# Kernel tuning notes

Hardware: AMD Instinct MI355X
Metric: run time of the kernel (lower is better)

The kernel has to match this reference:

```python
import jax, jax.numpy as jnp
import numpy as np

B, L, D, H = 2, 2048, 1024, 16
Dh = D // H            # 64
DIL = 2                # dilation
WIN = 256              # window_size
HID = 4 * D            # ffn hidden (mlp_ratio=4.0)
EPS = 1e-5             # LayerNorm eps (torch default)


def _layernorm(x, w, b):
    m = jnp.mean(x, axis=-1, keepdims=True)
    v = jnp.mean(jnp.square(x - m), axis=-1, keepdims=True)
    return (x - m) * jax.lax.rsqrt(v + EPS) * w + b


def _dilated_mask(L):
    i = jnp.arange(L)[:, None]
    j = jnp.arange(L)[None, :]
    d = i - j
    return (jnp.remainder(d, DIL) == 0) & (jnp.abs(d) <= WIN) & (j <= i)  # [L,L] bool, True=allowed


def setup_inputs() -> dict:
    key = jax.random.key(0)
    ks = jax.random.split(key, 16)
    s = 0.02
    return {
        "x": jax.random.normal(ks[0], (B, L, D), jnp.float32),
        "norm1_w": jnp.ones((D,), jnp.float32),
        "norm1_b": jnp.zeros((D,), jnp.float32),
        "qkv_w": jax.random.normal(ks[1], (D, 3 * D), jnp.float32) * s,
        "qkv_b": jnp.zeros((3 * D,), jnp.float32),
        "out_w": jax.random.normal(ks[2], (D, D), jnp.float32) * s,
        "out_b": jnp.zeros((D,), jnp.float32),
        "norm2_w": jnp.ones((D,), jnp.float32),
        "norm2_b": jnp.zeros((D,), jnp.float32),
        "ffn_w1": jax.random.normal(ks[3], (D, HID), jnp.float32) * s,
        "ffn_b1": jnp.zeros((HID,), jnp.float32),
        "ffn_w2": jax.random.normal(ks[4], (HID, D), jnp.float32) * s,
        "ffn_b2": jnp.zeros((D,), jnp.float32),
    }


def reference(x, norm1_w, norm1_b, qkv_w, qkv_b, out_w, out_b,
              norm2_w, norm2_b, ffn_w1, ffn_b1, ffn_w2, ffn_b2):
    # pre-norm dilated attention block
    xn = _layernorm(x, norm1_w, norm1_b)
    qkv = xn @ qkv_w + qkv_b                         # [B,L,3D]
    q, k, v = jnp.split(qkv, 3, axis=-1)
    to_h = lambda t: t.reshape(B, L, H, Dh).transpose(0, 2, 1, 3)  # [B,H,L,Dh]
    qh, kh, vh = to_h(q), to_h(k), to_h(v)

    scale = 1.0 / jnp.sqrt(jnp.float32(Dh))
    scores = jnp.einsum('bhqd,bhkd->bhqk', qh, kh) * scale  # [B,H,L,L]
    allowed = _dilated_mask(L)                               # [L,L]
    scores = jnp.where(allowed[None, None], scores, jnp.float32(-1e30))
    p = jax.nn.softmax(scores, axis=-1)
    o = jnp.einsum('bhqk,bhkd->bhqd', p, vh)                 # [B,H,L,Dh]
    o = o.transpose(0, 2, 1, 3).reshape(B, L, D)
    attn_out = o @ out_w + out_b

    y = x + attn_out                                          # residual (dropout=0)
    h = _layernorm(y, norm2_w, norm2_b)
    h = jax.nn.gelu(h @ ffn_w1 + ffn_b1, approximate=False) @ ffn_w2 + ffn_b2
    return y + h
```

## Files before the change

### kernel.cpp

```cpp
#include <hip/hip_runtime.h>
#include <math.h>

#define BB 2
#define LL 2048
#define DD 1024
#define HH 16
#define DH 64
#define HID 4096
#define MROWS (BB*LL)

typedef __attribute__((ext_vector_type(8))) short bf16x8;
typedef __attribute__((ext_vector_type(4))) float f32x4;

__device__ __forceinline__ unsigned short f2bf(float f) {
    unsigned u = __builtin_bit_cast(unsigned, f);
    unsigned r = u + 0x7fffu + ((u >> 16) & 1u);
    return (unsigned short)(r >> 16);
}

__device__ __forceinline__ void ldsload16(const void* g, void* l) {
    __builtin_amdgcn_global_load_lds(
        (const __attribute__((address_space(1))) unsigned int*)g,
        (__attribute__((address_space(3))) unsigned int*)l,
        16, 0, 0);
}

__global__ __launch_bounds__(256) void convT_kernel(const float* __restrict__ in,
                                                    unsigned short* __restrict__ out,
                                                    int K, int N) {
    __shared__ float tile[64][65];
    int kt = blockIdx.y << 6, nt = blockIdx.x << 6;
    int t = threadIdx.x;
    int tr = t >> 4;
    int tc = (t & 15) << 2;
    #pragma unroll
    for (int i = 0; i < 4; ++i) {
        float4 v = *reinterpret_cast<const float4*>(&in[(size_t)(kt + i*16 + tr) * N + nt + tc]);
        tile[i*16 + tr][tc+0] = v.x;
        tile[i*16 + tr][tc+1] = v.y;
        tile[i*16 + tr][tc+2] = v.z;
        tile[i*16 + tr][tc+3] = v.w;
    }
    __syncthreads();
    #pragma unroll
    for (int i = 0; i < 4; ++i) {
        int n = i*16 + tr;
        ushort4 o4;
        o4.x = f2bf(tile[tc+0][n]);
        o4.y = f2bf(tile[tc+1][n]);
        o4.z = f2bf(tile[tc+2][n]);
        o4.w = f2bf(tile[tc+3][n]);
        *reinterpret_cast<ushort4*>(&out[(size_t)(nt + n) * K + kt + tc]) = o4;
    }
}

__global__ __launch_bounds__(256) void ln_kernel(const float* __restrict__ in,
                                                 const float* __restrict__ w,
                                                 const float* __restrict__ b,
                                                 unsigned short* __restrict__ out) {
    int row = blockIdx.x;
    const float* x = in + (size_t)row * DD;
    unsigned short* o = out + (size_t)row * DD;
    int t = threadIdx.x;
    float4 v = reinterpret_cast<const float4*>(x)[t];
    float s  = v.x + v.y + v.z + v.w;
    float ss = v.x*v.x + v.y*v.y + v.z*v.z + v.w*v.w;
    #pragma unroll
    for (int off = 32; off > 0; off >>= 1) {
        s  += __shfl_down(s,  off, 64);
        ss += __shfl_down(ss, off, 64);
    }
    __shared__ float red[8];
    int wid = t >> 6, lane = t & 63;
    if (lane == 0) { red[wid] = s; red[4 + wid] = ss; }
    __syncthreads();
    if (t == 0) {
        float S  = red[0] + red[1] + red[2] + red[3];
        float SS = red[4] + red[5] + red[6] + red[7];
        float mean = S / DD;
        float var  = SS / DD - mean * mean;
        red[0] = mean;
        red[1] = rsqrtf(var + 1e-5f);
    }
    __syncthreads();
    float mean = red[0], rstd = red[1];
    float4 wv = reinterpret_cast<const float4*>(w)[t];
    float4 bv = reinterpret_cast<const float4*>(b)[t];
    ushort4 ov;
    ov.x = f2bf((v.x - mean) * rstd * wv.x + bv.x);
    ov.y = f2bf((v.y - mean) * rstd * wv.y + bv.y);
    ov.z = f2bf((v.z - mean) * rstd * wv.z + bv.z);
    ov.w = f2bf((v.w - mean) * rstd * wv.w + bv.w);
    reinterpret_cast<ushort4*>(o)[t] = ov;
}

template<int EPI>
__global__ __launch_bounds__(256) void mgemm(
    const unsigned short* __restrict__ A,
    const unsigned short* __restrict__ WT,
    const float* __restrict__ bias,
    const float* res, void* Cv,
    int M, int N, int K, int nbx)
{
    __shared__ __align__(16) unsigned char smem[49152];
    int bid = blockIdx.x;
    int nwg = gridDim.x;
    int cpx = nwg >> 3;
    int swz = (bid & 7) * cpx + (bid >> 3);
    int bn = (swz % nbx) * 128;
    int bm = (swz / nbx) * 128;
    int t = threadIdx.x, lane = t & 63, w = t >> 6;
    int wr = w >> 1, wc = w & 1;
    int l15 = lane & 15, l4 = lane >> 4;

    const unsigned short* Ap = A  + (size_t)(bm + w*32 + l15) * K + 8*l4;
    const unsigned short* Bp = WT + (size_t)(bn + w*32 + l15) * K + 8*l4;
    unsigned stoff = w*2048 + lane*16;

    f32x4 acc[4][4] = {};
    int nk = K >> 5;

    unsigned char* pb0 = smem;
    unsigned char* pb1 = smem + 16384;
    unsigned char* pb2 = smem + 32768;

    auto stage = [&](unsigned char* bs) {
        ldsload16(Ap,        bs + stoff);
        ldsload16(Ap + 16*K, bs + stoff + 1024);
        ldsload16(Bp,        bs + 8192 + stoff);
        ldsload16(Bp + 16*K, bs + 8192 + stoff + 1024);
        Ap += 32; Bp += 32;
    };

    stage(pb0);
    stage(pb1);

    for (int k = 0; k < nk; ++k) {
        if (k + 2 < nk) {
            stage(pb2);
            asm volatile("s_waitcnt vmcnt(8)\ns_barrier" ::: "memory");
        } else if (k + 2 == nk) {
            asm volatile("s_waitcnt vmcnt(4)\ns_barrier" ::: "memory");
        } else {
            asm volatile("s_waitcnt vmcnt(0)\ns_barrier" ::: "memory");
        }
        unsigned char* Asb = pb0;
        unsigned char* Bsb = pb0 + 8192;
        bf16x8 af[4], bfr[4];
        #pragma unroll
        for (int mm = 0; mm < 4; ++mm)
            af[mm] = *reinterpret_cast<const bf16x8*>(Asb + (wr*4 + mm)*1024 + lane*16);
        #pragma unroll
        for (int nn = 0; nn < 4; ++nn)
            bfr[nn] = *reinterpret_cast<const bf16x8*>(Bsb + (wc*4 + nn)*1024 + lane*16);
        #pragma unroll
        for (int mm = 0; mm < 4; ++mm)
            #pragma unroll
            for (int nn = 0; nn < 4; ++nn)
                acc[mm][nn] = __builtin_amdgcn_mfma_f32_16x16x32_bf16(af[mm], bfr[nn], acc[mm][nn], 0, 0, 0);
        asm volatile("s_waitcnt lgkmcnt(0)\ns_barrier" ::: "memory");
        unsigned char* tp = pb0; pb0 = pb1; pb1 = pb2; pb2 = tp;
    }

    #pragma unroll
    for (int mm = 0; mm < 4; ++mm) {
        int row0 = bm + wr*64 + mm*16 + l4*4;
        #pragma unroll
        for (int nn = 0; nn < 4; ++nn) {
            int col = bn + wc*64 + nn*16 + l15;
            float bi = bias[col];
            #pragma unroll
            for (int r = 0; r < 4; ++r) {
                float v = acc[mm][nn][r] + bi;
                size_t idx = (size_t)(row0 + r) * N + col;
                if (EPI == 2) {
                    ((float*)Cv)[idx] = v + res[idx];
                } else {
                    v = 0.5f * v * (1.0f + erff(v * 0.70710678118654752f));
                    ((unsigned short*)Cv)[idx] = f2bf(v);
                }
            }
        }
    }
}

template<int EPI>
__global__ __launch_bounds__(512, 2) void mgemm256(
    const unsigned short* __restrict__ A,
    const unsigned short* __restrict__ WT,
    const float* __restrict__ bias,
    void* Cv,
    unsigned short* __restrict__ vt,
    int M, int N, int K, int nbx)
{
    __shared__ __align__(16) unsigned char smem[131072];
    int bid = blockIdx.x;
    int nwg = gridDim.x;
    int cpx = nwg >> 3;
    int swz = (bid & 7) * cpx + (bid >> 3);
    int bn = (swz % nbx) * 256;
    int bm = (swz / nbx) * 256;
    int t = threadIdx.x, lane = t & 63, w = t >> 6;
    int wr = w >> 2, wc = w & 3;
    int l15 = lane & 15, l4 = lane >> 4;

    const unsigned short* Ap0 = A  + (size_t)(bm + w*16 + l15) * K + 8*l4;
    const unsigned short* Ap1 = Ap0 + (size_t)128 * K;
    const unsigned short* Bp0 = WT + (size_t)(bn + w*16 + l15) * K + 8*l4;
    const unsigned short* Bp1 = Bp0 + (size_t)128 * K;
    unsigned aoff = w*1024 + lane*16;
    int koff = 0;

    f32x4 acc[8][4] = {};
    int nk = K >> 6;

    auto stage = [&](int buf) {
        unsigned char* Asb = smem + (buf << 16);
        unsigned char* Bsb = Asb + 32768;
        ldsload16(Ap0 + koff,      Asb + aoff);
        ldsload16(Ap1 + koff,      Asb + aoff + 8192);
        ldsload16(Ap0 + koff + 32, Asb + aoff + 16384);
        ldsload16(Ap1 + koff + 32, Asb + aoff + 24576);
        ldsload16(Bp0 + koff,      Bsb + aoff);
        ldsload16(Bp1 + koff,      Bsb + aoff + 8192);
        ldsload16(Bp0 + koff + 32, Bsb + aoff + 16384);
        ldsload16(Bp1 + koff + 32, Bsb + aoff + 24576);
        koff += 64;
    };

    stage(0);
    for (int k = 0; k < nk; ++k) {
        if (k + 1 < nk) {
            stage((k + 1) & 1);
            asm volatile("s_waitcnt vmcnt(8)\ns_barrier" ::: "memory");
        } else {
            asm volatile("s_waitcnt vmcnt(0)\ns_barrier" ::: "memory");
        }
        unsigned char* Asb = smem + ((k & 1) << 16);
        unsigned char* Bsb = Asb + 32768;
        #pragma unroll
        for (int kc = 0; kc < 2; ++kc) {
            bf16x8 af[8], bfr[4];
            #pragma unroll
            for (int mm = 0; mm < 8; ++mm)
                af[mm] = *reinterpret_cast<const bf16x8*>(Asb + kc*16384 + (wr*8 + mm)*1024 + lane*16);
            #pragma unroll
            for (int nn = 0; nn < 4; ++nn)
                bfr[nn] = *reinterpret_cast<const bf16x8*>(Bsb + kc*16384 + (wc*4 + nn)*1024 + lane*16);
            #pragma unroll
            for (int mm = 0; mm < 8; ++mm)
                #pragma unroll
                for (int nn = 0; nn < 4; ++nn)
                    acc[mm][nn] = __builtin_amdgcn_mfma_f32_16x16x32_bf16(af[mm], bfr[nn], acc[mm][nn], 0, 0, 0);
        }
        asm volatile("s_waitcnt lgkmcnt(0)\ns_barrier" ::: "memory");
    }

    bool isv = (EPI == 3) && (bn >= 2048);
    #pragma unroll
    for (int mm = 0; mm < 8; ++mm) {
        int row0 = bm + wr*128 + mm*16 + l4*4;
        #pragma unroll
        for (int nn = 0; nn < 4; ++nn) {
            int col = bn + wc*64 + nn*16 + l15;
            float bi = bias[col];
            #pragma unroll
            for (int r = 0; r < 4; ++r) {
                float v = acc[mm][nn][r] + bi;
                int row = row0 + r;
                size_t idx = (size_t)row * N + col;
                if (EPI == 1) {
                    v = 0.5f * v * (1.0f + erff(v * 0.70710678118654752f));
                    ((unsigned short*)Cv)[idx] = f2bf(v);
                } else {
                    if (!isv) {
                        ((unsigned short*)Cv)[idx] = f2bf(v);
                    } else {
                        int bb = row >> 11, l = row & 2047;
                        int c2 = col - 2048, hh = c2 >> 6, dd = c2 & 63;
                        vt[((((size_t)(bb*HH + hh)*2 + (l & 1))*64 + dd) << 10) + (l >> 1)] = f2bf(v);
                    }
                }
            }
        }
    }
}

__global__ __launch_bounds__(64, 1) void mattn(
    const unsigned short* __restrict__ qkvb,
    const unsigned short* __restrict__ vt,
    unsigned short* __restrict__ o)
{
    __shared__ __align__(16) unsigned char PlB[8192];
    int qt = blockIdx.x, p = blockIdx.y, bh = blockIdx.z;
    int b = bh >> 4, h = bh & 15;
    int lane = threadIdx.x;
    int l15 = lane & 15, l4 = lane >> 4;

    bf16x8 qf[4][2];
    #pragma unroll
    for (int qb = 0; qb < 4; ++qb) {
        int tq = qt*64 + qb*16 + l15;
        const unsigned short* qr = qkvb + (size_t)(b*LL + 2*tq + p)*3072 + h*64 + 8*l4;
        qf[qb][0] = *reinterpret_cast<const bf16x8*>(qr);
        qf[qb][1] = *reinterpret_cast<const bf16x8*>(qr + 32);
    }

    float mreg[4], lreg[4];
    #pragma unroll
    for (int qb = 0; qb < 4; ++qb) { mreg[qb] = -1e30f; lreg[qb] = 0.f; }
    f32x4 oac[4][4] = {};

    const unsigned short* vbase = vt + ((size_t)((b*HH + h)*2 + p) << 16);

    int kt0 = qt - 2; if (kt0 < 0) kt0 = 0;
    for (int kt = kt0; kt <= qt; ++kt) {
        bf16x8 kf[4][2], vf[4][2];
        #pragma unroll
        for (int kb = 0; kb < 4; ++kb) {
            const unsigned short* kr = qkvb + (size_t)(b*LL + 2*(kt*64 + kb*16 + l15) + p)*3072 + 1024 + h*64 + 8*l4;
            kf[kb][0] = *reinterpret_cast<const bf16x8*>(kr);
            kf[kb][1] = *reinterpret_cast<const bf16x8*>(kr + 32);
        }
        #pragma unroll
        for (int mt = 0; mt < 4; ++mt) {
            const unsigned short* vr = vbase + (mt*16 + l15)*1024 + kt*64 + 8*l4;
            vf[mt][0] = *reinterpret_cast<const bf16x8*>(vr);
            vf[mt][1] = *reinterpret_cast<const bf16x8*>(vr + 32);
        }
        f32x4 st[4][4];
        #pragma unroll
        for (int kb = 0; kb < 4; ++kb)
            #pragma unroll
            for (int qb = 0; qb < 4; ++qb) {
                f32x4 z = {0.f, 0.f, 0.f, 0.f};
                z = __builtin_amdgcn_mfma_f32_16x16x32_bf16(kf[kb][0], qf[qb][0], z, 0, 0, 0);
                st[kb][qb] = __builtin_amdgcn_mfma_f32_16x16x32_bf16(kf[kb][1], qf[qb][1], z, 0, 0, 0);
            }
        #pragma unroll
        for (int qb = 0; qb < 4; ++qb) {
            int tq = qt*64 + qb*16 + l15;
            int q = qb*16 + l15;
            float tmax = -1e30f;
            #pragma unroll
            for (int kb = 0; kb < 4; ++kb)
                #pragma unroll
                for (int r = 0; r < 4; ++r) {
                    int kc = kt*64 + kb*16 + 4*l4 + r;
                    float sv = st[kb][qb][r] * 0.125f;
                    sv = (kc + 128 >= tq && kc <= tq) ? sv : -1e30f;
                    st[kb][qb][r] = sv;
                    tmax = fmaxf(tmax, sv);
                }
            tmax = fmaxf(tmax, __shfl_xor(tmax, 16, 64));
            tmax = fmaxf(tmax, __shfl_xor(tmax, 32, 64));
            float newm = fmaxf(mreg[qb], tmax);
            float corr = __expf(mreg[qb] - newm);
            mreg[qb] = newm;
            float ps = 0.f;
            #pragma unroll
            for (int kb = 0; kb < 4; ++kb) {
                float p0 = __expf(st[kb][qb][0] - newm);
                float p1 = __expf(st[kb][qb][1] - newm);
                float p2 = __expf(st[kb][qb][2] - newm);
                float p3 = __expf(st[kb][qb][3] - newm);
                ps += (p0 + p1) + (p2 + p3);
                unsigned lo = (unsigned)f2bf(p0) | ((unsigned)f2bf(p1) << 16);
                unsigned hi = (unsigned)f2bf(p2) | ((unsigned)f2bf(p3) << 16);
                unsigned byteoff = ((unsigned)(q << 7) + (unsigned)(kb*32 + 8*l4)) ^ ((unsigned)(q & 7) << 4);
                *reinterpret_cast<uint2*>(PlB + byteoff) = make_uint2(lo, hi);
            }
            ps += __shfl_xor(ps, 16, 64);
            ps += __shfl_xor(ps, 32, 64);
            lreg[qb] = lreg[qb] * corr + ps;
            #pragma unroll
            for (int mt = 0; mt < 4; ++mt) {
                oac[mt][qb][0] *= corr; oac[mt][qb][1] *= corr;
                oac[mt][qb][2] *= corr; oac[mt][qb][3] *= corr;
            }
        }
        #pragma unroll
        for (int c = 0; c < 2; ++c)
            #pragma unroll
            for (int qb = 0; qb < 4; ++qb) {
                int q = qb*16 + l15;
                unsigned rb = ((unsigned)(q << 7) + (unsigned)(c*64 + 16*l4)) ^ ((unsigned)(q & 7) << 4);
                bf16x8 pf = *reinterpret_cast<const bf16x8*>(PlB + rb);
                #pragma unroll
                for (int mt = 0; mt < 4; ++mt)
                    oac[mt][qb] = __builtin_amdgcn_mfma_f32_16x16x32_bf16(vf[mt][c], pf, oac[mt][qb], 0, 0, 0);
            }
    }

    #pragma unroll
    for (int qb = 0; qb < 4; ++qb) {
        float inv = 1.f / lreg[qb];
        int tq = qt*64 + qb*16 + l15;
        unsigned short* orow = o + (size_t)(b*LL + 2*tq + p)*DD + h*64;
        #pragma unroll
        for (int mt = 0; mt < 4; ++mt) {
            int d0 = mt*16 + 4*l4;
            ushort4 o4;
            o4.x = f2bf(oac[mt][qb][0] * inv);
            o4.y = f2bf(oac[mt][qb][1] * inv);
            o4.z = f2bf(oac[mt][qb][2] * inv);
            o4.w = f2bf(oac[mt][qb][3] * inv);
            *reinterpret_cast<ushort4*>(orow + d0) = o4;
        }
    }
}

extern "C" void kernel_launch(void* const* d_in, const int* in_sizes, int n_in,
                              void* d_out, int out_size, void* d_ws, size_t ws_size,
                              hipStream_t stream) {
    const float* x      = (const float*)d_in[0];
    const float* n1w    = (const float*)d_in[1];
    const float* n1b    = (const float*)d_in[2];
    const float* qkv_w  = (const float*)d_in[3];
    const float* qkv_b  = (const float*)d_in[4];
    const float* out_w  = (const float*)d_in[5];
    const float* out_b  = (const float*)d_in[6];
    const float* n2w    = (const float*)d_in[7];
    const float* n2b    = (const float*)d_in[8];
    const float* ffn_w1 = (const float*)d_in[9];
    const float* ffn_b1 = (const float*)d_in[10];
    const float* ffn_w2 = (const float*)d_in[11];
    const float* ffn_b2 = (const float*)d_in[12];

    unsigned char* wsb = (unsigned char*)d_ws;
    const size_t MB = 1024 * 1024;

    unsigned short* qkvb = (unsigned short*)wsb;
    unsigned short* vt   = (unsigned short*)(wsb + 24*MB);
    unsigned short* mid  = (unsigned short*)wsb;
    unsigned short* o_b  = (unsigned short*)(wsb + 32*MB);
    unsigned short* xn   = (unsigned short*)(wsb + 40*MB);
    unsigned short* hbuf = (unsigned short*)(wsb + 48*MB);
    unsigned short* qkvT = (unsigned short*)(wsb + 56*MB);
    unsigned short* outT = (unsigned short*)(wsb + 62*MB);
    unsigned short* w1T  = (unsigned short*)(wsb + 64*MB);
    unsigned short* w2T  = (unsigned short*)(wsb + 72*MB);
    float*          y    = (float*)d_out;

    convT_kernel<<<dim3(3*DD/64, DD/64), 256, 0, stream>>>(qkv_w,  qkvT, DD,  3*DD);
    convT_kernel<<<dim3(DD/64,   DD/64), 256, 0, stream>>>(out_w,  outT, DD,  DD);
    convT_kernel<<<dim3(HID/64,  DD/64), 256, 0, stream>>>(ffn_w1, w1T,  DD,  HID);
    convT_kernel<<<dim3(DD/64,  HID/64), 256, 0, stream>>>(ffn_w2, w2T,  HID, DD);

    ln_kernel<<<MROWS, 256, 0, stream>>>(x, n1w, n1b, xn);
    mgemm256<3><<<(3*DD/256)*(MROWS/256), 512, 0, stream>>>(
        xn, qkvT, qkv_b, qkvb, vt, MROWS, 3*DD, DD, 3*DD/256);
    mattn<<<dim3(16, 2, BB*HH), 64, 0, stream>>>(qkvb, vt, o_b);
    mgemm<2><<<(DD/128)*(MROWS/128), 256, 0, stream>>>(
        o_b, outT, out_b, x, y, MROWS, DD, DD, DD/128);
    ln_kernel<<<MROWS, 256, 0, stream>>>(y, n2w, n2b, hbuf);
    mgemm256<1><<<(HID/256)*(MROWS/256), 512, 0, stream>>>(
        hbuf, w1T, ffn_b1, mid, nullptr, MROWS, HID, DD, HID/256);
    mgemm<2><<<(DD/128)*(MROWS/128), 256, 0, stream>>>(
        mid, w2T, ffn_b2, y, y, MROWS, DD, HID, DD/128);
}
```

Before: 388.3 us.

## Split-K the out-projection and FFN2 GEMMs, fusing partial reduction into LayerNorm

The two N=1024 GEMMs (the attention out-projection and FFN down-projection) each split K in half, launching twice as many workgroups so the GPU's compute units are better filled. The first K-half writes bias plus residual plus its partial sum. The second half writes a raw fp32 partial to freed workspace. For the out-projection, the partial is added inside a new fused LayerNorm kernel that also updates y. For FFN2, a separate float4 add kernel folds the partial in. This trades extra fp32 partial-buffer traffic and one more launch for higher GEMM occupancy and shorter per-block K loops.

```diff
diff --git a/kernel.cpp b/kernel.cpp
--- a/kernel.cpp
+++ b/kernel.cpp
@@ -94,31 +94,93 @@
     reinterpret_cast<ushort4*>(o)[t] = ov;
 }
 
-template<int EPI>
-__global__ __launch_bounds__(256) void mgemm(
+__global__ __launch_bounds__(256) void ln_fuse_kernel(float* __restrict__ y,
+                                                      const float* __restrict__ part,
+                                                      const float* __restrict__ w,
+                                                      const float* __restrict__ b,
+                                                      unsigned short* __restrict__ out) {
+    int row = blockIdx.x;
+    float* xr = y + (size_t)row * DD;
+    const float* pr = part + (size_t)row * DD;
+    unsigned short* o = out + (size_t)row * DD;
+    int t = threadIdx.x;
+    float4 v  = reinterpret_cast<float4*>(xr)[t];
+    float4 pv = reinterpret_cast<const float4*>(pr)[t];
+    v.x += pv.x; v.y += pv.y; v.z += pv.z; v.w += pv.w;
+    reinterpret_cast<float4*>(xr)[t] = v;
+    float s  = v.x + v.y + v.z + v.w;
+    float ss = v.x*v.x + v.y*v.y + v.z*v.z + v.w*v.w;
+    #pragma unroll
+    for (int off = 32; off > 0; off >>= 1) {
+        s  += __shfl_down(s,  off, 64);
+        ss += __shfl_down(ss, off, 64);
+    }
+    __shared__ float red[8];
+    int wid = t >> 6, lane = t & 63;
+    if (lane == 0) { red[wid] = s; red[4 + wid] = ss; }
+    __syncthreads();
+    if (t == 0) {
+        float S  = red[0] + red[1] + red[2] + red[3];
+        float SS = red[4] + red[5] + red[6] + red[7];
+        float mean = S / DD;
+        float var  = SS / DD - mean * mean;
+        red[0] = mean;
+        red[1] = rsqrtf(var + 1e-5f);
+    }
+    __syncthreads();
+    float mean = red[0], rstd = red[1];
+    float4 wv = reinterpret_cast<const float4*>(w)[t];
+    float4 bv = reinterpret_cast<const float4*>(b)[t];
+    ushort4 ov;
+    ov.x = f2bf((v.x - mean) * rstd * wv.x + bv.x);
+    ov.y = f2bf((v.y - mean) * rstd * wv.y + bv.y);
+    ov.z = f2bf((v.z - mean) * rstd * wv.z + bv.z);
+    ov.w = f2bf((v.w - mean) * rstd * wv.w + bv.w);
+    reinterpret_cast<ushort4*>(o)[t] = ov;
+}
+
+__global__ __launch_bounds__(256) void fadd_kernel(float* __restrict__ y,
+                                                   const float* __restrict__ p, int n4) {
+    int i = blockIdx.x * 256 + threadIdx.x;
+    int stride = gridDim.x * 256;
+    for (; i < n4; i += stride) {
+        float4 a = reinterpret_cast<float4*>(y)[i];
+        float4 b = reinterpret_cast<const float4*>(p)[i];
+        a.x += b.x; a.y += b.y; a.z += b.z; a.w += b.w;
+        reinterpret_cast<float4*>(y)[i] = a;
+    }
+}
+
+template<int SK>
+__global__ __launch_bounds__(256) void mgemm_sk(
     const unsigned short* __restrict__ A,
     const unsigned short* __restrict__ WT,
     const float* __restrict__ bias,
-    const float* res, void* Cv,
+    const float* __restrict__ res,
+    float* __restrict__ C,
+    float* __restrict__ part,
     int M, int N, int K, int nbx)
 {
     __shared__ __align__(16) unsigned char smem[49152];
+    int half = gridDim.x / SK;
     int bid = blockIdx.x;
-    int nwg = gridDim.x;
-    int cpx = nwg >> 3;
-    int swz = (bid & 7) * cpx + (bid >> 3);
+    int sk = (SK > 1) ? (bid / half) : 0;
+    int rel = bid - sk * half;
+    int cpx = half >> 3;
+    int swz = (rel & 7) * cpx + (rel >> 3);
     int bn = (swz % nbx) * 128;
     int bm = (swz / nbx) * 128;
+    int Keff = K / SK;
     int t = threadIdx.x, lane = t & 63, w = t >> 6;
     int wr = w >> 1, wc = w & 1;
     int l15 = lane & 15, l4 = lane >> 4;
 
-    const unsigned short* Ap = A  + (size_t)(bm + w*32 + l15) * K + 8*l4;
-    const unsigned short* Bp = WT + (size_t)(bn + w*32 + l15) * K + 8*l4;
+    const unsigned short* Ap = A  + (size_t)(bm + w*32 + l15) * K + sk*Keff + 8*l4;
+    const unsigned short* Bp = WT + (size_t)(bn + w*32 + l15) * K + sk*Keff + 8*l4;
     unsigned stoff = w*2048 + lane*16;
 
     f32x4 acc[4][4] = {};
-    int nk = K >> 5;
+    int nk = Keff >> 5;
 
     unsigned char* pb0 = smem;
     unsigned char* pb1 = smem + 16384;
@@ -171,13 +233,11 @@
             float bi = bias[col];
             #pragma unroll
             for (int r = 0; r < 4; ++r) {
-                float v = acc[mm][nn][r] + bi;
                 size_t idx = (size_t)(row0 + r) * N + col;
-                if (EPI == 2) {
-                    ((float*)Cv)[idx] = v + res[idx];
+                if (sk == 0) {
+                    C[idx] = acc[mm][nn][r] + bi + res[idx];
                 } else {
-                    v = 0.5f * v * (1.0f + erff(v * 0.70710678118654752f));
-                    ((unsigned short*)Cv)[idx] = f2bf(v);
+                    part[idx] = acc[mm][nn][r];
                 }
             }
         }
@@ -430,17 +490,19 @@
     unsigned char* wsb = (unsigned char*)d_ws;
     const size_t MB = 1024 * 1024;
 
-    unsigned short* qkvb = (unsigned short*)wsb;
-    unsigned short* vt   = (unsigned short*)(wsb + 24*MB);
-    unsigned short* mid  = (unsigned short*)wsb;
-    unsigned short* o_b  = (unsigned short*)(wsb + 32*MB);
-    unsigned short* xn   = (unsigned short*)(wsb + 40*MB);
-    unsigned short* hbuf = (unsigned short*)(wsb + 48*MB);
-    unsigned short* qkvT = (unsigned short*)(wsb + 56*MB);
-    unsigned short* outT = (unsigned short*)(wsb + 62*MB);
-    unsigned short* w1T  = (unsigned short*)(wsb + 64*MB);
-    unsigned short* w2T  = (unsigned short*)(wsb + 72*MB);
-    float*          y    = (float*)d_out;
+    unsigned short* qkvb  = (unsigned short*)wsb;
+    unsigned short* vt    = (unsigned short*)(wsb + 24*MB);
+    unsigned short* mid   = (unsigned short*)wsb;
+    float*          part1a= (float*)wsb;
+    unsigned short* o_b   = (unsigned short*)(wsb + 32*MB);
+    float*          part1b= (float*)(wsb + 32*MB);
+    unsigned short* xn    = (unsigned short*)(wsb + 40*MB);
+    unsigned short* hbuf  = (unsigned short*)(wsb + 48*MB);
+    unsigned short* qkvT  = (unsigned short*)(wsb + 56*MB);
+    unsigned short* outT  = (unsigned short*)(wsb + 62*MB);
+    unsigned short* w1T   = (unsigned short*)(wsb + 64*MB);
+    unsigned short* w2T   = (unsigned short*)(wsb + 72*MB);
+    float*          y     = (float*)d_out;
 
     convT_kernel<<<dim3(3*DD/64, DD/64), 256, 0, stream>>>(qkv_w,  qkvT, DD,  3*DD);
     convT_kernel<<<dim3(DD/64,   DD/64), 256, 0, stream>>>(out_w,  outT, DD,  DD);
@@ -451,11 +513,12 @@
     mgemm256<3><<<(3*DD/256)*(MROWS/256), 512, 0, stream>>>(
         xn, qkvT, qkv_b, qkvb, vt, MROWS, 3*DD, DD, 3*DD/256);
     mattn<<<dim3(16, 2, BB*HH), 64, 0, stream>>>(qkvb, vt, o_b);
-    mgemm<2><<<(DD/128)*(MROWS/128), 256, 0, stream>>>(
-        o_b, outT, out_b, x, y, MROWS, DD, DD, DD/128);
-    ln_kernel<<<MROWS, 256, 0, stream>>>(y, n2w, n2b, hbuf);
+    mgemm_sk<2><<<2*(DD/128)*(MROWS/128), 256, 0, stream>>>(
+        o_b, outT, out_b, x, y, part1a, MROWS, DD, DD, DD/128);
+    ln_fuse_kernel<<<MROWS, 256, 0, stream>>>(y, part1a, n2w, n2b, hbuf);
     mgemm256<1><<<(HID/256)*(MROWS/256), 512, 0, stream>>>(
         hbuf, w1T, ffn_b1, mid, nullptr, MROWS, HID, DD, HID/256);
-    mgemm<2><<<(DD/128)*(MROWS/128), 256, 0, stream>>>(
-        mid, w2T, ffn_b2, y, y, MROWS, DD, HID, DD/128);
-}
+    mgemm_sk<2><<<2*(DD/128)*(MROWS/128), 256, 0, stream>>>(
+        mid, w2T, ffn_b2, y, y, part1b, MROWS, DD, HID, DD/128);
+    fadd_kernel<<<2048, 256, 0, stream>>>(y, part1b, MROWS*DD/4);
+}
```

Measured after the change: 404.7 us. 1.04x slower.
